# Optimization experiments

Hardware: AMD Instinct MI355X
Metric: run time of the kernel (lower is better)

## Reference

```python
import jax, jax.numpy as jnp
import numpy as np

H = 8            # heads
M = 256          # num_landmarks
PINV_ITERS = 6
PAD = 16         # residual_conv_kernel(33)//2


def layernorm(x, g, b, eps=1e-5):
    mu = x.mean(-1, keepdims=True)
    var = ((x - mu) ** 2).mean(-1, keepdims=True)
    return (x - mu) * jax.lax.rsqrt(var + eps) * g + b


def moore_penrose_pinv(x, iters=PINV_ITERS):
    # iterative Moore-Penrose pseudo-inverse (Nystromformer)
    abs_x = jnp.abs(x)
    col = abs_x.sum(-1)
    row = abs_x.sum(-2)
    z = jnp.swapaxes(x, -1, -2) / (jnp.max(col) * jnp.max(row))
    eye = jnp.eye(x.shape[-1], dtype=x.dtype)
    for _ in range(iters):
        xz = x @ z
        z = 0.25 * z @ (13.0 * eye - xz @ (15.0 * eye - xz @ (7.0 * eye - xz)))
    return z


def attn_block(y, ln1_g, ln1_b, w_qkv, w_out, b_out, res_w,
               ln2_g, ln2_b, w1, b1, w2, b2):
    B, N, D = y.shape
    inner = w_qkv.shape[1] // 3
    dh = inner // H
    xn = layernorm(y, ln1_g, ln1_b)
    qkv = xn @ w_qkv                      # [B,N,3*inner]
    q, k, v = jnp.split(qkv, 3, axis=-1)
    to_heads = lambda t: t.reshape(B, N, H, dh).transpose(0, 2, 1, 3)  # [B,H,N,dh]
    q, k, v = map(to_heads, (q, k, v))
    q = q * (dh ** -0.5)
    l = N // M                            # tokens per landmark (N % M == 0 here)
    q_l = q.reshape(B, H, M, l, dh).mean(3)  # sum/l == mean -> [B,H,M,dh]
    k_l = k.reshape(B, H, M, l, dh).mean(3)
    attn1 = jax.nn.softmax(jnp.einsum('bhnd,bhmd->bhnm', q, k_l), axis=-1)
    attn2 = jax.nn.softmax(jnp.einsum('bhid,bhjd->bhij', q_l, k_l), axis=-1)
    attn3 = jax.nn.softmax(jnp.einsum('bhmd,bhnd->bhmn', q_l, k), axis=-1)
    attn2_inv = moore_penrose_pinv(attn2)
    out = (attn1 @ attn2_inv) @ (attn3 @ v)   # [B,H,N,dh]
    # depthwise residual conv over sequence dim: v as NCHW with C=H, Hdim=N, Wdim=dh
    res = jax.lax.conv_general_dilated(
        v, res_w, window_strides=(1, 1), padding=[(PAD, PAD), (0, 0)],
        dimension_numbers=('NCHW', 'OIHW', 'NCHW'), feature_group_count=H)
    out = out + res
    out = out.transpose(0, 2, 1, 3).reshape(B, N, inner)
    y = y + out @ w_out + b_out
    yn = layernorm(y, ln2_g, ln2_b)
    hdn = jax.nn.gelu(yn @ w1 + b1, approximate=False)
    return y + hdn @ w2 + b2


def setup_inputs() -> dict:
    key = jax.random.key(0)
    ks = jax.random.split(key, 8)
    B, N, D, NB = 4, 4096, 256, 2
    inner = D
    p = lambda k, shp: jax.random.normal(k, shp, jnp.float32) * 0.02
    return {
        'x': jax.random.normal(ks[0], (B, N, D), jnp.float32),
        'ln1_g': jnp.ones((NB, D), jnp.float32),
        'ln1_b': jnp.zeros((NB, D), jnp.float32),
        'w_qkv': p(ks[1], (NB, D, 3 * inner)),
        'w_out': p(ks[2], (NB, inner, D)),
        'b_out': jnp.zeros((NB, D), jnp.float32),
        'res_w': p(ks[3], (NB, H, 1, 33, 1)),
        'ln2_g': jnp.ones((NB, D), jnp.float32),
        'ln2_b': jnp.zeros((NB, D), jnp.float32),
        'w1': p(ks[4], (NB, D, 2 * D)),
        'b1': jnp.zeros((NB, 2 * D), jnp.float32),
        'w2': p(ks[5], (NB, 2 * D, D)),
        'b2': jnp.zeros((NB, D), jnp.float32),
    }


def reference(x, ln1_g, ln1_b, w_qkv, w_out, b_out, res_w,
              ln2_g, ln2_b, w1, b1, w2, b2):
    y = x
    for i in range(ln1_g.shape[0]):
        y = attn_block(y, ln1_g[i], ln1_b[i], w_qkv[i], w_out[i], b_out[i],
                       res_w[i], ln2_g[i], ln2_b[i], w1[i], b1[i], w2[i], b2[i])
    return y
```

## Files before the change

kernel.cpp:

```cpp
#include <hip/hip_runtime.h>
#include <math.h>

typedef float f32x4 __attribute__((ext_vector_type(4)));
typedef short s16x8 __attribute__((ext_vector_type(8)));
typedef unsigned short u16;
typedef unsigned int u32;

#define MFMA16(a,b,c) __builtin_amdgcn_mfma_f32_16x16x32_bf16((a),(b),(c),0,0,0)
#define AS1 __attribute__((address_space(1)))
#define AS3 __attribute__((address_space(3)))

__device__ __forceinline__ void dma16(const u16* g, u16* l){
  __builtin_amdgcn_global_load_lds((const AS1 u32*)g, (AS3 u32*)l, 16, 0, 0);
}

__device__ __forceinline__ float bf2f(u16 u){
  union { unsigned int i; float f; } v; v.i = ((unsigned int)u)<<16; return v.f;
}
__device__ __forceinline__ u16 f2bf(float f){
  union { float f; unsigned int i; } v; v.f = f;
  unsigned int x = v.i;
  return (u16)((x + 0x7fffu + ((x>>16)&1u))>>16);
}

enum { EPI_QKV=0, EPI_PINV=1, EPI_BIAS_RES=2, EPI_BIAS_GELU=3 };

template<int EPI>
__global__ __launch_bounds__(256)
void kgemm(const u16* __restrict__ A, const u16* __restrict__ BT, int K, int lda, int ldb,
           const float* __restrict__ bias, const float* __restrict__ base,
           float* __restrict__ resout,
           u16* __restrict__ outb, int ldc)
{
  __shared__ __align__(16) u16 As[128*32];
  __shared__ __align__(16) u16 Bs[64*32];
  const int tid = threadIdx.x;
  const int w = tid>>6, l = tid&63, q = l>>4, ln = l&15;
  const int m0 = blockIdx.x*128, n0 = blockIdx.y*64;
  const int lrow = l>>2, lch = l&3;

  f32x4 acc[2][4];
  #pragma unroll
  for (int i=0;i<2;i++)
    #pragma unroll
    for (int j=0;j<4;j++){ acc[i][j][0]=0.f; acc[i][j][1]=0.f; acc[i][j][2]=0.f; acc[i][j][3]=0.f; }

  for (int k0=0; k0<K; k0+=32){
    #pragma unroll
    for (int c=0;c<2;c++){
      int row = 32*w + 16*c + lrow;
      int gch = lch ^ ((row>>1)&3);
      dma16(A + (long)(m0+row)*lda + k0 + gch*8, &As[(32*w+16*c)*32]);
    }
    {
      int row = 16*w + lrow;
      int gch = lch ^ ((row>>1)&3);
      dma16(BT + (long)(n0+row)*ldb + k0 + gch*8, &Bs[(16*w)*32]);
    }
    __syncthreads();
    s16x8 af[2], bfr[4];
    #pragma unroll
    for (int mt=0;mt<2;mt++){
      int row = w*32 + mt*16 + ln;
      af[mt] = *(const s16x8*)&As[row*32 + ((q ^ ((row>>1)&3))<<3)];
    }
    #pragma unroll
    for (int nt=0;nt<4;nt++){
      int row = nt*16 + ln;
      bfr[nt] = *(const s16x8*)&Bs[row*32 + ((q ^ ((row>>1)&3))<<3)];
    }
    #pragma unroll
    for (int mt=0;mt<2;mt++)
      #pragma unroll
      for (int nt=0;nt<4;nt++)
        acc[mt][nt] = MFMA16(af[mt], bfr[nt], acc[mt][nt]);
    __syncthreads();
  }

  #pragma unroll
  for (int mt=0;mt<2;mt++)
  #pragma unroll
  for (int nt=0;nt<4;nt++)
  #pragma unroll
  for (int r=0;r<4;r++){
    int mrow = m0 + w*32 + mt*16 + q*4 + r;
    int ncol = n0 + nt*16 + ln;
    float v = acc[mt][nt][r];
    if (EPI==EPI_BIAS_RES){
      long idx = (long)mrow*ldc + ncol;
      resout[idx] = base[idx] + v + bias[ncol];
    } else {
      outb[(long)mrow*ldc + ncol] = f2bf(v);
    }
  }
}

template<int EPI>
__global__ __launch_bounds__(256)
void kgemm2(const u16* __restrict__ A, const u16* __restrict__ BT, int K, int lda, int ldb,
            const float* __restrict__ bias, u16* __restrict__ outb, int ldc,
            u16* __restrict__ qo, u16* __restrict__ ko, u16* __restrict__ vo,
            u16* __restrict__ qlm, u16* __restrict__ klm)
{
  __shared__ __align__(16) u16 As[128*32];
  __shared__ __align__(16) u16 Bs[128*32];
  const int tid = threadIdx.x;
  const int w = tid>>6, wy = w>>1, wx = w&1, l = tid&63, q = l>>4, ln = l&15;
  const int m0 = blockIdx.x*128, n0 = blockIdx.y*128;
  const int lrow = l>>2, lch = l&3;

  f32x4 acc[4][4];
  #pragma unroll
  for (int i=0;i<4;i++)
    #pragma unroll
    for (int j=0;j<4;j++){ acc[i][j][0]=0.f; acc[i][j][1]=0.f; acc[i][j][2]=0.f; acc[i][j][3]=0.f; }

  for (int k0=0; k0<K; k0+=32){
    #pragma unroll
    for (int c=0;c<2;c++){
      int row = 32*w + 16*c + lrow;
      int gch = lch ^ ((row>>1)&3);
      dma16(A + (long)(m0+row)*lda + k0 + gch*8, &As[(32*w+16*c)*32]);
      dma16(BT + (long)(n0+row)*ldb + k0 + gch*8, &Bs[(32*w+16*c)*32]);
    }
    __syncthreads();
    s16x8 af[4], bfr[4];
    #pragma unroll
    for (int mt=0;mt<4;mt++){
      int row = wy*64 + mt*16 + ln;
      af[mt] = *(const s16x8*)&As[row*32 + ((q ^ ((row>>1)&3))<<3)];
    }
    #pragma unroll
    for (int nt=0;nt<4;nt++){
      int row = wx*64 + nt*16 + ln;
      bfr[nt] = *(const s16x8*)&Bs[row*32 + ((q ^ ((row>>1)&3))<<3)];
    }
    #pragma unroll
    for (int mt=0;mt<4;mt++)
      #pragma unroll
      for (int nt=0;nt<4;nt++)
        acc[mt][nt] = MFMA16(af[mt], bfr[nt], acc[mt][nt]);
    __syncthreads();
  }

  #pragma unroll
  for (int mt=0;mt<4;mt++)
  #pragma unroll
  for (int nt=0;nt<4;nt++){
    int ncol = n0 + wx*64 + nt*16 + ln;
    if (EPI==EPI_QKV){
      int sel = ncol>>8, hd = ncol&255, h = hd>>5, d = hd&31;
      u16* dst = sel==0 ? qo : (sel==1 ? ko : vo);
      float sc2 = (sel==0) ? 0.17677669529663689f : 1.f;
      float s = 0.f;
      #pragma unroll
      for (int r=0;r<4;r++){
        int mrow = m0 + wy*64 + mt*16 + q*4 + r;
        int b = mrow>>12, n = mrow&4095;
        float v = acc[mt][nt][r]*sc2;
        dst[(((long)(b*8+h)*4096 + n)<<5) + d] = f2bf(v);
        s += v;
      }
      if (sel < 2){
        s += __shfl_xor(s, 16);
        s += __shfl_xor(s, 32);
        if (q == 0){
          int mrow0 = m0 + wy*64 + mt*16;
          int b = mrow0>>12, grp = (mrow0&4095)>>4;
          u16* ldst = (sel==0) ? qlm : klm;
          ldst[(((long)(b*8+h)*256 + grp)<<5) + d] = f2bf(s*(1.0f/16.0f));
        }
      }
    } else {
      #pragma unroll
      for (int r=0;r<4;r++){
        int mrow = m0 + wy*64 + mt*16 + q*4 + r;
        float x = acc[mt][nt][r] + bias[ncol];
        float g = 0.5f*x*(1.0f + erff(x*0.70710678118654752f));
        outb[(long)mrow*ldc + ncol] = f2bf(g);
      }
    }
  }
}

__device__ __forceinline__ int swidx(int row, int col){
  int cc = col>>3;
  int sl = (cc&24)|((cc&7)^((row>>1)&7));
  return row*256 + sl*8 + (col&7);
}

__device__ __forceinline__ void stage256(const u16* __restrict__ g, u16* lds, int w, int l){
  const int drow = l>>5, dch = l&31;
  #pragma unroll
  for (int c=0;c<32;c++){
    int base = (c*4 + w)*2;
    int row = base + drow;
    int gch = (dch&24) | ((dch&7) ^ ((row>>1)&7));
    dma16(g + (long)row*256 + gch*8, &lds[base*256]);
  }
}

__device__ __forceinline__ void stage32(const u16* __restrict__ g, u16* lds, int w, int l){
  const int drow = l>>5, dch = l&31;
  #pragma unroll
  for (int c=0;c<4;c++){
    int base = (c*4 + w)*2;
    int row = base + drow;
    int gch = (dch&24) | ((dch&7) ^ ((row>>1)&7));
    dma16(g + (long)row*256 + gch*8, &lds[base*256]);
  }
}

__device__ __forceinline__ void mult32(const u16* aL, int arow0, const u16* bL,
                                       int w, int l, f32x4 (&acc)[2][4]){
  const int q=l>>4, ln=l&15, wn0=w*64;
  #pragma unroll
  for (int mt=0;mt<2;mt++)
    #pragma unroll
    for (int nt=0;nt<4;nt++){ acc[mt][nt][0]=0.f; acc[mt][nt][1]=0.f; acc[mt][nt][2]=0.f; acc[mt][nt][3]=0.f; }
  #pragma unroll
  for (int kq=0;kq<8;kq++){
    int ca = kq*4+q;
    s16x8 af[2];
    #pragma unroll
    for (int mt=0;mt<2;mt++){
      int r = arow0 + mt*16 + ln;
      af[mt] = *(const s16x8*)&aL[r*256 + (((ca&24)|((ca&7)^((r>>1)&7)))<<3)];
    }
    #pragma unroll
    for (int nt=0;nt<4;nt++){
      int n = wn0 + nt*16 + ln;
      s16x8 bfr = *(const s16x8*)&bL[n*256 + (((ca&24)|((ca&7)^((n>>1)&7)))<<3)];
      acc[0][nt] = MFMA16(af[0], bfr, acc[0][nt]);
      acc[1][nt] = MFMA16(af[1], bfr, acc[1][nt]);
    }
  }
}

__device__ __forceinline__ void polyinit13(const u16* aL, int arow0, int w, int l, f32x4 (&poly)[2][4]){
  const int q=l>>4, ln=l&15, wn0=w*64;
  #pragma unroll
  for (int mt=0;mt<2;mt++)
  #pragma unroll
  for (int nt=0;nt<4;nt++)
  #pragma unroll
  for (int r=0;r<4;r++){
    int row = arow0 + mt*16 + q*4 + r;
    int col = wn0 + nt*16 + ln;
    poly[mt][nt][r] = 13.f*bf2f(aL[swidx(row,col)]);
  }
}

__device__ __forceinline__ void polyaxpy(f32x4 (&poly)[2][4], const f32x4 (&acc)[2][4], float sc){
  #pragma unroll
  for (int mt=0;mt<2;mt++)
    #pragma unroll
    for (int nt=0;nt<4;nt++)
      #pragma unroll
      for (int r=0;r<4;r++) poly[mt][nt][r] += sc*acc[mt][nt][r];
}

__device__ __forceinline__ void writeT(u16* Ts, const f32x4 (&acc)[2][4], int w, int l, float sc){
  const int q=l>>4, ln=l&15, wn0=w*64;
  #pragma unroll
  for (int mt=0;mt<2;mt++)
  #pragma unroll
  for (int nt=0;nt<4;nt++)
  #pragma unroll
  for (int r=0;r<4;r++){
    int row = mt*16 + q*4 + r;
    int col = wn0 + nt*16 + ln;
    Ts[swidx(row,col)] = f2bf(sc*acc[mt][nt][r]);
  }
}

__device__ __forceinline__ void epi_poly(u16* __restrict__ out, int rowbase,
                                         const f32x4 (&poly)[2][4], int w, int l, float sc){
  const int q=l>>4, ln=l&15, wn0=w*64;
  #pragma unroll
  for (int mt=0;mt<2;mt++)
  #pragma unroll
  for (int nt=0;nt<4;nt++)
  #pragma unroll
  for (int r=0;r<4;r++){
    int row = rowbase + mt*16 + q*4 + r;
    int col = wn0 + nt*16 + ln;
    out[(long)row*256 + col] = f2bf(sc*poly[mt][nt][r]);
  }
}

__global__ __launch_bounds__(256)
void kw0(const float* __restrict__ cs_p, float* __restrict__ scal,
         const float* __restrict__ num_p, const float* __restrict__ den_p,
         const u16* __restrict__ X, u16* __restrict__ W0, u16* __restrict__ h0)
{
  __shared__ __align__(16) u16 Wf[65536];
  __shared__ __align__(16) u16 Ts[8192];
  const int tid=threadIdx.x, w=tid>>6, l=tid&63;
  const int bid=blockIdx.x, xcd=bid&7, j=bid>>3;
  const int batch = xcd*4 + (j>>3), slab = j&7;

  stage256(X + (long)batch*65536, Wf, w, l);

  float* red = (float*)Ts;
  float mx = 0.f;
  for (int i=tid;i<8192;i+=256){
    float s = 0.f;
    #pragma unroll
    for (int c=0;c<8;c++) s += cs_p[(long)c*8192 + i];
    mx = fmaxf(mx, s);
  }
  red[tid] = mx; __syncthreads();
  for (int s=128;s>0;s>>=1){ if (tid<s) red[tid] = fmaxf(red[tid], red[tid+s]); __syncthreads(); }
  float s0 = 1.0f/red[0];
  if (bid==0 && tid==0) scal[0] = s0;

  f32x4 acc[2][4];
  mult32(Wf, slab*32, Wf, w, l, acc);
  {
    const int q=l>>4, ln=l&15, wn0=w*64;
    u16* ob = W0 + (long)batch*65536;
    #pragma unroll
    for (int mt=0;mt<2;mt++)
    #pragma unroll
    for (int nt=0;nt<4;nt++)
    #pragma unroll
    for (int r=0;r<4;r++){
      int row = slab*32 + mt*16 + q*4 + r;
      int col = wn0 + nt*16 + ln;
      ob[(long)row*256 + col] = f2bf(acc[mt][nt][r]*s0);
    }
  }

  if (slab==0){
    __syncthreads();
    float (*lt)[257] = (float(*)[257])Wf;
    for (int i=tid;i<8192;i+=256){
      int m = i>>5, d = i&31;
      float sn = 0.f, sd = 0.f;
      #pragma unroll
      for (int c=0;c<8;c++){
        sn += num_p[((long)(c*32+batch))*8192 + i];
        sd += den_p[(c*32+batch)*256 + m];
      }
      lt[d][m] = sn/sd;
    }
    __syncthreads();
    u16* o = h0 + (long)batch*8192;
    for (int j2=tid;j2<8192;j2+=256){
      int d = j2>>8, m = j2&255;
      o[j2] = f2bf(lt[d][m]);
    }
  }
}

__global__ __launch_bounds__(256)
void kiter(const u16* __restrict__ Win, u16* __restrict__ Wout,
           const u16* __restrict__ hin, u16* __restrict__ hout)
{
  __shared__ __align__(16) u16 Wf[65536];
  __shared__ __align__(16) u16 Ts[8192];
  const int tid=threadIdx.x, w=tid>>6, l=tid&63;
  const int bid=blockIdx.x, xcd=bid&7, j=bid>>3;
  const int batch = xcd*4 + (j>>3), slab = j&7;

  stage256(Win + (long)batch*65536, Wf, w, l);
  __syncthreads();

  f32x4 acc[2][4], poly[2][4];
  polyinit13(Wf, slab*32, w, l, poly);
  mult32(Wf, slab*32, Wf, w, l, acc);
  polyaxpy(poly, acc, -15.f);
  writeT(Ts, acc, w, l, 1.f);
  __syncthreads();
  mult32(Ts, 0, Wf, w, l, acc);
  polyaxpy(poly, acc, 7.f);
  __syncthreads();
  writeT(Ts, acc, w, l, 1.f);
  __syncthreads();
  mult32(Ts, 0, Wf, w, l, acc);
  polyaxpy(poly, acc, -1.f);
  epi_poly(Wout + (long)batch*65536, slab*32, poly, w, l, 0.25f);

  if (slab==0){
    __syncthreads();
    stage32(hin + (long)batch*8192, Ts, w, l);
    __syncthreads();
    polyinit13(Ts, 0, w, l, poly);
    mult32(Ts, 0, Wf, w, l, acc);
    polyaxpy(poly, acc, -15.f);
    __syncthreads(); writeT(Ts, acc, w, l, 1.f); __syncthreads();
    mult32(Ts, 0, Wf, w, l, acc);
    polyaxpy(poly, acc, 7.f);
    __syncthreads(); writeT(Ts, acc, w, l, 1.f); __syncthreads();
    mult32(Ts, 0, Wf, w, l, acc);
    polyaxpy(poly, acc, -1.f);
    epi_poly(hout + (long)batch*8192, 0, poly, w, l, 0.25f);
  }
}

__global__ __launch_bounds__(256)
void ktail(const u16* __restrict__ W5, const u16* __restrict__ h5,
           const u16* __restrict__ XT, const float* __restrict__ scal,
           u16* __restrict__ uT)
{
  __shared__ __align__(16) u16 Wf[65536];
  __shared__ __align__(16) u16 Ts[8192];
  const int tid=threadIdx.x, w=tid>>6, l=tid&63;
  const int batch = blockIdx.x;

  stage256(W5 + (long)batch*65536, Wf, w, l);
  stage32(h5 + (long)batch*8192, Ts, w, l);
  __syncthreads();

  f32x4 acc[2][4], poly[2][4];
  polyinit13(Ts, 0, w, l, poly);
  mult32(Ts, 0, Wf, w, l, acc);
  polyaxpy(poly, acc, -15.f);
  __syncthreads(); writeT(Ts, acc, w, l, 1.f); __syncthreads();
  mult32(Ts, 0, Wf, w, l, acc);
  polyaxpy(poly, acc, 7.f);
  __syncthreads(); writeT(Ts, acc, w, l, 1.f); __syncthreads();
  mult32(Ts, 0, Wf, w, l, acc);
  polyaxpy(poly, acc, -1.f);
  __syncthreads();
  writeT(Ts, poly, w, l, 0.25f);
  __syncthreads();
  stage256(XT + (long)batch*65536, Wf, w, l);
  __syncthreads();
  mult32(Ts, 0, Wf, w, l, acc);
  const float s0 = scal[0];
  {
    const int q=l>>4, ln=l&15, wn0=w*64;
    u16* ob = uT + (long)batch*8192;
    #pragma unroll
    for (int mt=0;mt<2;mt++)
    #pragma unroll
    for (int nt=0;nt<4;nt++)
    #pragma unroll
    for (int r=0;r<4;r++){
      int row = mt*16 + q*4 + r;
      int col = wn0 + nt*16 + ln;
      ob[(long)row*256 + col] = f2bf(acc[mt][nt][r]*s0);
    }
  }
}

__global__ __launch_bounds__(256)
void kln(const float* __restrict__ y, const float* __restrict__ g, const float* __restrict__ b,
         u16* __restrict__ out)
{
  int w = threadIdx.x>>6, l = threadIdx.x&63;
  long row = (long)blockIdx.x*4 + w;
  float4 v = ((const float4*)(y + row*256))[l];
  float s = v.x+v.y+v.z+v.w;
  #pragma unroll
  for (int m=1;m<64;m<<=1) s += __shfl_xor(s, m);
  float mu = s*(1.0f/256.0f);
  float dx=v.x-mu, dy=v.y-mu, dz=v.z-mu, dw=v.w-mu;
  float s2 = dx*dx+dy*dy+dz*dz+dw*dw;
  #pragma unroll
  for (int m=1;m<64;m<<=1) s2 += __shfl_xor(s2, m);
  float rs = rsqrtf(s2*(1.0f/256.0f) + 1e-5f);
  float4 gg = ((const float4*)g)[l];
  float4 bb = ((const float4*)b)[l];
  ushort4 o;
  o.x = f2bf(dx*rs*gg.x + bb.x);
  o.y = f2bf(dy*rs*gg.y + bb.y);
  o.z = f2bf(dz*rs*gg.z + bb.z);
  o.w = f2bf(dw*rs*gg.w + bb.w);
  *(ushort4*)(out + row*256 + l*4) = o;
}

__global__ __launch_bounds__(256)
void kattn23(const u16* __restrict__ ql, const u16* __restrict__ kl,
             u16* __restrict__ X, u16* __restrict__ XT, float* __restrict__ cs_p,
             const u16* __restrict__ kk, const u16* __restrict__ vv,
             float* __restrict__ num_p, float* __restrict__ den_p)
{
  __shared__ __align__(16) u16 Pbuf[4][64][40];
  __shared__ __align__(16) u16 vT[32][40];
  __shared__ float qrow[32][33];
  __shared__ float psum[32][4];
  __shared__ float rsum[32];
  int bh = blockIdx.y;
  int tid = threadIdx.x, w = tid>>6, l = tid&63, q = l>>4, ln = l&15;

  if (blockIdx.x < 8){
    int r0 = blockIdx.x*32;
    int c = tid;
    #pragma unroll
    for (int i=0;i<4;i++){
      int e = c*4+i; int rr = e>>5, dd = e&31;
      qrow[rr][dd] = bf2f(ql[((long)bh*256 + r0+rr)*32 + dd]);
    }
    float kc[32];
    {
      const u16* kp = kl + ((long)bh*256 + c)*32;
      #pragma unroll
      for (int d=0;d<32;d++) kc[d] = bf2f(kp[d]);
    }
    __syncthreads();
    float er[32]; float colacc = 0.f;
    for (int r=0;r<32;r++){
      float s = 0.f;
      #pragma unroll
      for (int d=0;d<32;d++) s += qrow[r][d]*kc[d];
      float e = __expf(s);
      er[r] = e;
      float wsum = e;
      #pragma unroll
      for (int m=1;m<64;m<<=1) wsum += __shfl_xor(wsum, m);
      if (l==0) psum[r][w] = wsum;
    }
    __syncthreads();
    if (c<32) rsum[c] = psum[c][0]+psum[c][1]+psum[c][2]+psum[c][3];
    __syncthreads();
    for (int r=0;r<32;r++){
      float x = er[r]/rsum[r];
      u16 xb = f2bf(x);
      X [((long)bh*256 + r0+r)*256 + c] = xb;
      XT[((long)bh*256 + c)*256 + r0+r] = xb;
      colacc += x;
    }
    cs_p[(long)blockIdx.x*8192 + bh*256 + c] = colacc;
    return;
  }

  int chunk = blockIdx.x - 8;
  f32x4 z4; z4[0]=0.f; z4[1]=0.f; z4[2]=0.f; z4[3]=0.f;
  f32x4 acc[4][2]; f32x4 dacc[4];
  #pragma unroll
  for (int mt=0;mt<4;mt++){ dacc[mt]=z4; acc[mt][0]=z4; acc[mt][1]=z4; }
  const u16* qlb = ql + (long)bh*8192;
  const u16* kb  = kk + (long)bh*131072;
  const u16* vb  = vv + (long)bh*131072;
  int vn = tid>>3, vd = (tid&7)*4;
  for (int s=0;s<16;s++){
    int n0 = chunk*512 + s*32;
    ushort4 vx = *(const ushort4*)(vb + (long)(n0+vn)*32 + vd);
    vT[vd+0][vn]=vx.x; vT[vd+1][vn]=vx.y; vT[vd+2][vn]=vx.z; vT[vd+3][vn]=vx.w;
    __syncthreads();
    s16x8 bk[2];
    #pragma unroll
    for (int nt=0;nt<2;nt++) bk[nt] = *(const s16x8*)(kb + (long)(n0 + nt*16 + ln)*32 + q*8);
    #pragma unroll
    for (int mt=0;mt<4;mt++){
      s16x8 aq = *(const s16x8*)(qlb + (long)(w*64 + mt*16 + ln)*32 + q*8);
      #pragma unroll
      for (int nt=0;nt<2;nt++){
        f32x4 sf = MFMA16(aq, bk[nt], z4);
        f32x4 ef;
        #pragma unroll
        for (int r=0;r<4;r++) ef[r] = __expf(sf[r]);
        dacc[mt] += ef;
        #pragma unroll
        for (int r=0;r<4;r++) Pbuf[w][mt*16 + q*4 + r][nt*16 + ln] = f2bf(ef[r]);
      }
    }
    #pragma unroll
    for (int mt=0;mt<4;mt++){
      s16x8 ap = *(const s16x8*)&Pbuf[w][mt*16 + ln][q*8];
      #pragma unroll
      for (int nt=0;nt<2;nt++){
        s16x8 bv = *(const s16x8*)&vT[nt*16 + ln][q*8];
        acc[mt][nt] = MFMA16(ap, bv, acc[mt][nt]);
      }
    }
    __syncthreads();
  }
  #pragma unroll
  for (int mt=0;mt<4;mt++)
    #pragma unroll
    for (int r=0;r<4;r++){
      float x = dacc[mt][r];
      x += __shfl_xor(x,1); x += __shfl_xor(x,2); x += __shfl_xor(x,4); x += __shfl_xor(x,8);
      dacc[mt][r] = x;
    }
  long pbase = (long)(chunk*32 + bh);
  #pragma unroll
  for (int mt=0;mt<4;mt++)
    #pragma unroll
    for (int nt=0;nt<2;nt++)
      #pragma unroll
      for (int r=0;r<4;r++){
        int mg = w*64 + mt*16 + q*4 + r;
        num_p[pbase*8192 + (long)mg*32 + nt*16 + ln] = acc[mt][nt][r];
      }
  if (ln==0){
    #pragma unroll
    for (int mt=0;mt<4;mt++)
      #pragma unroll
      for (int r=0;r<4;r++)
        den_p[pbase*256 + w*64 + mt*16 + q*4 + r] = dacc[mt][r];
  }
}

__global__ __launch_bounds__(256)
void kattn1u(const u16* __restrict__ qq, const u16* __restrict__ kl, const u16* __restrict__ uT,
             const u16* __restrict__ vv, const float* __restrict__ rw,
             u16* __restrict__ aoutb)
{
  int nch = blockIdx.x, bh = blockIdx.y;
  int b = bh>>3, h = bh&7;
  int tid = threadIdx.x, w = tid>>6, l = tid&63, q = l>>4, ln = l&15;
  __shared__ __align__(16) u16 Pbuf[4][32][40];
  __shared__ __align__(16) u16 vtile[160][36];
  int r0g = nch*128;
  const u16* vb = vv + (long)bh*131072;
  #pragma unroll
  for (int it=0; it<5; it++){
    int slot = tid + it*256;
    int rr = slot>>3, c = (slot&7)*4;
    int s = r0g - 16 + rr;
    ushort4 val; val.x=0; val.y=0; val.z=0; val.w=0;
    if (s>=0 && s<4096) val = *(const ushort4*)(vb + (long)s*32 + c);
    *(ushort4*)&vtile[rr][c] = val;
  }
  __syncthreads();

  f32x4 z4; z4[0]=0.f; z4[1]=0.f; z4[2]=0.f; z4[3]=0.f;
  f32x4 acc[2][2]; f32x4 dacc[2];
  #pragma unroll
  for (int mt=0;mt<2;mt++){ dacc[mt]=z4; acc[mt][0]=z4; acc[mt][1]=z4; }
  const u16* qb  = qq + (long)bh*131072;
  const u16* klb = kl + (long)bh*8192;
  const u16* ub  = uT + (long)bh*8192;
  int r0 = r0g + w*32;
  for (int s=0;s<8;s++){
    s16x8 bk[2];
    #pragma unroll
    for (int nt=0;nt<2;nt++) bk[nt] = *(const s16x8*)(klb + (long)(s*32 + nt*16 + ln)*32 + q*8);
    #pragma unroll
    for (int mt=0;mt<2;mt++){
      s16x8 aq = *(const s16x8*)(qb + (long)(r0 + mt*16 + ln)*32 + q*8);
      #pragma unroll
      for (int nt=0;nt<2;nt++){
        f32x4 sf = MFMA16(aq, bk[nt], z4);
        f32x4 ef;
        #pragma unroll
        for (int r=0;r<4;r++) ef[r] = __expf(sf[r]);
        dacc[mt] += ef;
        #pragma unroll
        for (int r=0;r<4;r++) Pbuf[w][mt*16 + q*4 + r][nt*16 + ln] = f2bf(ef[r]);
      }
    }
    #pragma unroll
    for (int mt=0;mt<2;mt++){
      s16x8 ap = *(const s16x8*)&Pbuf[w][mt*16 + ln][q*8];
      #pragma unroll
      for (int nt=0;nt<2;nt++){
        s16x8 bu = *(const s16x8*)(ub + (long)(nt*16 + ln)*256 + s*32 + q*8);
        acc[mt][nt] = MFMA16(ap, bu, acc[mt][nt]);
      }
    }
  }
  #pragma unroll
  for (int mt=0;mt<2;mt++)
    #pragma unroll
    for (int r=0;r<4;r++){
      float x = dacc[mt][r];
      x += __shfl_xor(x,1); x += __shfl_xor(x,2); x += __shfl_xor(x,4); x += __shfl_xor(x,8);
      dacc[mt][r] = x;
    }

  const float* wp = rw + h*33;
  float w_[33];
  #pragma unroll
  for (int j=0;j<33;j++) w_[j] = wp[j];

  #pragma unroll
  for (int mt=0;mt<2;mt++){
    int nl = w*32 + mt*16 + q*4;
    #pragma unroll
    for (int nt=0;nt<2;nt++){
      int d = nt*16 + ln;
      float vvv[36];
      #pragma unroll
      for (int j=0;j<36;j++) vvv[j] = bf2f(vtile[nl + j][d]);
      #pragma unroll
      for (int r=0;r<4;r++){
        float cv = 0.f;
        #pragma unroll
        for (int j=0;j<33;j++) cv += w_[j]*vvv[r+j];
        int n = r0 + mt*16 + q*4 + r;
        long oidx = ((long)b*4096 + n)*256 + h*32 + d;
        aoutb[oidx] = f2bf(acc[mt][nt][r]/dacc[mt][r] + cv);
      }
    }
  }
}

__global__ __launch_bounds__(256)
void kcvtall(const float* __restrict__ wqkv, const float* __restrict__ wout,
             const float* __restrict__ w1, const float* __restrict__ w2,
             u16* __restrict__ wqkvT, u16* __restrict__ woutT,
             u16* __restrict__ w1T, u16* __restrict__ w2T)
{
  __shared__ float t[32][33];
  int z = blockIdx.x;
  const float* src; u16* dst; int K, Nn, bx, by;
  if (z < 384){      int i=z/192, r=z%192; src=wqkv+(long)i*196608; dst=wqkvT+(long)i*196608; K=256; Nn=768; bx=r%24; by=r/24; }
  else if (z < 512){ int zz=z-384; int i=zz/64, r=zz%64; src=wout+(long)i*65536; dst=woutT+(long)i*65536; K=256; Nn=256; bx=r%8; by=r/8; }
  else if (z < 768){ int zz=z-512; int i=zz/128, r=zz%128; src=w1+(long)i*131072; dst=w1T+(long)i*131072; K=256; Nn=512; bx=r%16; by=r/16; }
  else {             int zz=z-768; int i=zz/128, r=zz%128; src=w2+(long)i*131072; dst=w2T+(long)i*131072; K=512; Nn=256; bx=r%8; by=r/8; }
  int n0 = bx*32, k0 = by*32;
  int tx = threadIdx.x&31, ty = threadIdx.x>>5;
  #pragma unroll
  for (int i=0;i<4;i++) t[ty+i*8][tx] = src[(long)(k0+ty+i*8)*Nn + n0+tx];
  __syncthreads();
  #pragma unroll
  for (int i=0;i<4;i++) dst[(long)(n0+ty+i*8)*K + k0+tx] = f2bf(t[tx][ty+i*8]);
}

extern "C" void kernel_launch(void* const* d_in, const int* in_sizes, int n_in,
                              void* d_out, int out_size, void* d_ws, size_t ws_size,
                              hipStream_t stream)
{
  const float* x    = (const float*)d_in[0];
  const float* ln1g = (const float*)d_in[1];
  const float* ln1b = (const float*)d_in[2];
  const float* wqkv = (const float*)d_in[3];
  const float* wout = (const float*)d_in[4];
  const float* bout = (const float*)d_in[5];
  const float* resw = (const float*)d_in[6];
  const float* ln2g = (const float*)d_in[7];
  const float* ln2b = (const float*)d_in[8];
  const float* w1   = (const float*)d_in[9];
  const float* b1   = (const float*)d_in[10];
  const float* w2   = (const float*)d_in[11];
  const float* b2   = (const float*)d_in[12];
  float* y = (float*)d_out;
  char* ws = (char*)d_ws;

  u16* xn    = (u16*)(ws + 0);
  u16* qb    = (u16*)(ws + 8388608);
  u16* kb    = (u16*)(ws + 16777216);
  u16* vb    = (u16*)(ws + 25165824);
  u16* ql    = (u16*)(ws + 33554432);
  u16* kl    = (u16*)(ws + 34078720);
  u16* X     = (u16*)(ws + 34603008);
  u16* XT    = (u16*)(ws + 38797312);
  u16* h0b   = (u16*)(ws + 42991616);
  u16* WA    = (u16*)(ws + 51380224);
  u16* WB    = (u16*)(ws + 55574528);
  u16* hA    = (u16*)(ws + 68157440);
  u16* hB    = (u16*)(ws + 72351744);
  float* num_p = (float*)(ws + 76546048);
  float* den_p = (float*)(ws + 84934656);
  float* cs_p  = (float*)(ws + 85196800);
  float* scal  = (float*)(ws + 85458944);
  u16* uT    = (u16*)(ws + 85459200);
  u16* aoutb = (u16*)(ws + 85983488);
  u16* wqkvT = (u16*)(ws + 94372096);
  u16* woutT = (u16*)(ws + 95158528);
  u16* w1T   = (u16*)(ws + 95420672);
  u16* w2T   = (u16*)(ws + 95944960);
  u16* hdn   = (u16*)(ws + 51380224);

  (void)in_sizes; (void)n_in; (void)out_size; (void)ws_size;

  kcvtall<<<1024,256,0,stream>>>(wqkv, wout, w1, w2, wqkvT, woutT, w1T, w2T);

  for (int i=0;i<2;i++){
    kln<<<4096,256,0,stream>>>(i==0 ? x : y, ln1g + i*256, ln1b + i*256, xn);
    kgemm2<EPI_QKV><<<dim3(128,6),256,0,stream>>>(xn, wqkvT + (long)i*196608, 256, 256, 256,
        nullptr, nullptr, 0, qb,kb,vb, ql,kl);
    kattn23<<<dim3(16,32),256,0,stream>>>(ql, kl, X, XT, cs_p, kb, vb, num_p, den_p);

    kw0<<<256,256,0,stream>>>(cs_p, scal, num_p, den_p, X, WA, h0b);
    u16 *Wi = WA, *Wo = WB, *hi = h0b, *ho = hA;
    for (int it=0; it<5; it++){
      kiter<<<256,256,0,stream>>>(Wi, Wo, hi, ho);
      u16* t = Wi; Wi = Wo; Wo = t;
      hi = ho; ho = (ho == hA) ? hB : hA;
    }
    ktail<<<32,256,0,stream>>>(Wi, hi, XT, scal, uT);

    kattn1u<<<dim3(32,32),256,0,stream>>>(qb, kl, uT, vb, resw + i*264, aoutb);
    kgemm<EPI_BIAS_RES><<<dim3(128,4),256,0,stream>>>(aoutb, woutT + (long)i*65536, 256,256,256,
        bout + i*256, i==0 ? x : y, y, nullptr, 256);
    kln<<<4096,256,0,stream>>>(y, ln2g + i*256, ln2b + i*256, xn);
    kgemm2<EPI_BIAS_GELU><<<dim3(128,4),256,0,stream>>>(xn, w1T + (long)i*131072, 256, 256, 256,
        b1 + i*512, hdn, 512, nullptr,nullptr,nullptr, nullptr,nullptr);
    kgemm<EPI_BIAS_RES><<<dim3(128,4),256,0,stream>>>(hdn, w2T + (long)i*131072, 512,512,512,
        b2 + i*256, y, y, nullptr, 256);
  }
}
```

Before: 542.6 us.

## Fuse layernorm into residual GEMM epilogues and widen pinv kernels to 512 threads

Replaces the bias+residual GEMM with a full-row (N=256) GEMM whose epilogue writes y and also computes the next layernorm, which removes the standalone layernorm launches. The first layernorm is folded into the weight-conversion kernel. The pinv iteration kernels now run with 512 threads and smaller per-wave tiles. Full-row tiles cut the GEMM grid to 128 blocks and raise register pressure (a 2x16 accumulator), which may reduce occupancy. On the last block, the second residual GEMM computes an unused layernorm using ln1 params index 1.

```diff
diff --git a/kernel.cpp b/kernel.cpp
--- a/kernel.cpp
+++ b/kernel.cpp
@@ -23,77 +23,7 @@
   return (u16)((x + 0x7fffu + ((x>>16)&1u))>>16);
 }
 
-enum { EPI_QKV=0, EPI_PINV=1, EPI_BIAS_RES=2, EPI_BIAS_GELU=3 };
-
-template<int EPI>
-__global__ __launch_bounds__(256)
-void kgemm(const u16* __restrict__ A, const u16* __restrict__ BT, int K, int lda, int ldb,
-           const float* __restrict__ bias, const float* __restrict__ base,
-           float* __restrict__ resout,
-           u16* __restrict__ outb, int ldc)
-{
-  __shared__ __align__(16) u16 As[128*32];
-  __shared__ __align__(16) u16 Bs[64*32];
-  const int tid = threadIdx.x;
-  const int w = tid>>6, l = tid&63, q = l>>4, ln = l&15;
-  const int m0 = blockIdx.x*128, n0 = blockIdx.y*64;
-  const int lrow = l>>2, lch = l&3;
-
-  f32x4 acc[2][4];
-  #pragma unroll
-  for (int i=0;i<2;i++)
-    #pragma unroll
-    for (int j=0;j<4;j++){ acc[i][j][0]=0.f; acc[i][j][1]=0.f; acc[i][j][2]=0.f; acc[i][j][3]=0.f; }
-
-  for (int k0=0; k0<K; k0+=32){
-    #pragma unroll
-    for (int c=0;c<2;c++){
-      int row = 32*w + 16*c + lrow;
-      int gch = lch ^ ((row>>1)&3);
-      dma16(A + (long)(m0+row)*lda + k0 + gch*8, &As[(32*w+16*c)*32]);
-    }
-    {
-      int row = 16*w + lrow;
-      int gch = lch ^ ((row>>1)&3);
-      dma16(BT + (long)(n0+row)*ldb + k0 + gch*8, &Bs[(16*w)*32]);
-    }
-    __syncthreads();
-    s16x8 af[2], bfr[4];
-    #pragma unroll
-    for (int mt=0;mt<2;mt++){
-      int row = w*32 + mt*16 + ln;
-      af[mt] = *(const s16x8*)&As[row*32 + ((q ^ ((row>>1)&3))<<3)];
-    }
-    #pragma unroll
-    for (int nt=0;nt<4;nt++){
-      int row = nt*16 + ln;
-      bfr[nt] = *(const s16x8*)&Bs[row*32 + ((q ^ ((row>>1)&3))<<3)];
-    }
-    #pragma unroll
-    for (int mt=0;mt<2;mt++)
-      #pragma unroll
-      for (int nt=0;nt<4;nt++)
-        acc[mt][nt] = MFMA16(af[mt], bfr[nt], acc[mt][nt]);
-    __syncthreads();
-  }
-
-  #pragma unroll
-  for (int mt=0;mt<2;mt++)
-  #pragma unroll
-  for (int nt=0;nt<4;nt++)
-  #pragma unroll
-  for (int r=0;r<4;r++){
-    int mrow = m0 + w*32 + mt*16 + q*4 + r;
-    int ncol = n0 + nt*16 + ln;
-    float v = acc[mt][nt][r];
-    if (EPI==EPI_BIAS_RES){
-      long idx = (long)mrow*ldc + ncol;
-      resout[idx] = base[idx] + v + bias[ncol];
-    } else {
-      outb[(long)mrow*ldc + ncol] = f2bf(v);
-    }
-  }
-}
+enum { EPI_QKV=0, EPI_BIAS_GELU=3 };
 
 template<int EPI>
 __global__ __launch_bounds__(256)
@@ -183,6 +113,110 @@
   }
 }
 
+__global__ __launch_bounds__(256)
+void kgemmLN(const u16* __restrict__ A, const u16* __restrict__ BT, int K,
+             const float* __restrict__ bias, const float* __restrict__ base,
+             float* __restrict__ yout,
+             const float* __restrict__ lng, const float* __restrict__ lnb,
+             u16* __restrict__ xnout)
+{
+  __shared__ __align__(16) u16 As[128*32];
+  __shared__ __align__(16) u16 Bs[256*32];
+  const int tid = threadIdx.x;
+  const int w = tid>>6, l = tid&63, q = l>>4, ln = l&15;
+  const int m0 = blockIdx.x*128;
+  const int lrow = l>>2, lch = l&3;
+
+  f32x4 acc[2][16];
+  #pragma unroll
+  for (int i=0;i<2;i++)
+    #pragma unroll
+    for (int j=0;j<16;j++){ acc[i][j][0]=0.f; acc[i][j][1]=0.f; acc[i][j][2]=0.f; acc[i][j][3]=0.f; }
+
+  for (int k0=0; k0<K; k0+=32){
+    #pragma unroll
+    for (int c=0;c<2;c++){
+      int row = 32*w + 16*c + lrow;
+      int gch = lch ^ ((row>>1)&3);
+      dma16(A + (long)(m0+row)*K + k0 + gch*8, &As[(32*w+16*c)*32]);
+    }
+    #pragma unroll
+    for (int c=0;c<4;c++){
+      int row = 64*w + 16*c + lrow;
+      int gch = lch ^ ((row>>1)&3);
+      dma16(BT + (long)row*K + k0 + gch*8, &Bs[(64*w+16*c)*32]);
+    }
+    __syncthreads();
+    s16x8 af[2];
+    #pragma unroll
+    for (int mt=0;mt<2;mt++){
+      int row = w*32 + mt*16 + ln;
+      af[mt] = *(const s16x8*)&As[row*32 + ((q ^ ((row>>1)&3))<<3)];
+    }
+    #pragma unroll
+    for (int nt=0;nt<16;nt++){
+      int row = nt*16 + ln;
+      s16x8 bfr = *(const s16x8*)&Bs[row*32 + ((q ^ ((row>>1)&3))<<3)];
+      acc[0][nt] = MFMA16(af[0], bfr, acc[0][nt]);
+      acc[1][nt] = MFMA16(af[1], bfr, acc[1][nt]);
+    }
+    __syncthreads();
+  }
+
+  float rb[16];
+  #pragma unroll
+  for (int nt=0;nt<16;nt++) rb[nt] = bias[nt*16 + ln];
+  #pragma unroll
+  for (int mt=0;mt<2;mt++)
+  #pragma unroll
+  for (int r=0;r<4;r++){
+    long rowb = (long)(m0 + w*32 + mt*16 + q*4 + r)*256;
+    #pragma unroll
+    for (int nt=0;nt<16;nt++){
+      int col = nt*16 + ln;
+      float v = base[rowb + col] + acc[mt][nt][r] + rb[nt];
+      acc[mt][nt][r] = v;
+      yout[rowb + col] = v;
+    }
+  }
+  float mu[2][4], rs[2][4];
+  #pragma unroll
+  for (int mt=0;mt<2;mt++)
+  #pragma unroll
+  for (int r=0;r<4;r++){
+    float s = 0.f;
+    #pragma unroll
+    for (int nt=0;nt<16;nt++) s += acc[mt][nt][r];
+    s += __shfl_xor(s,1); s += __shfl_xor(s,2); s += __shfl_xor(s,4); s += __shfl_xor(s,8);
+    mu[mt][r] = s*(1.0f/256.0f);
+  }
+  #pragma unroll
+  for (int mt=0;mt<2;mt++)
+  #pragma unroll
+  for (int r=0;r<4;r++){
+    float vs = 0.f;
+    #pragma unroll
+    for (int nt=0;nt<16;nt++){ float d = acc[mt][nt][r]-mu[mt][r]; vs += d*d; }
+    vs += __shfl_xor(vs,1); vs += __shfl_xor(vs,2); vs += __shfl_xor(vs,4); vs += __shfl_xor(vs,8);
+    rs[mt][r] = rsqrtf(vs*(1.0f/256.0f) + 1e-5f);
+  }
+  float rg[16], rbb[16];
+  #pragma unroll
+  for (int nt=0;nt<16;nt++){ int col = nt*16+ln; rg[nt]=lng[col]; rbb[nt]=lnb[col]; }
+  #pragma unroll
+  for (int mt=0;mt<2;mt++)
+  #pragma unroll
+  for (int r=0;r<4;r++){
+    long rowb = (long)(m0 + w*32 + mt*16 + q*4 + r)*256;
+    #pragma unroll
+    for (int nt=0;nt<16;nt++){
+      int col = nt*16 + ln;
+      float d = acc[mt][nt][r]-mu[mt][r];
+      xnout[rowb + col] = f2bf(d*rs[mt][r]*rg[nt] + rbb[nt]);
+    }
+  }
+}
+
 __device__ __forceinline__ int swidx(int row, int col){
   int cc = col>>3;
   int sl = (cc&24)|((cc&7)^((row>>1)&7));
@@ -192,8 +226,8 @@
 __device__ __forceinline__ void stage256(const u16* __restrict__ g, u16* lds, int w, int l){
   const int drow = l>>5, dch = l&31;
   #pragma unroll
-  for (int c=0;c<32;c++){
-    int base = (c*4 + w)*2;
+  for (int c=0;c<16;c++){
+    int base = (c*8 + w)*2;
     int row = base + drow;
     int gch = (dch&24) | ((dch&7) ^ ((row>>1)&7));
     dma16(g + (long)row*256 + gch*8, &lds[base*256]);
@@ -203,8 +237,8 @@
 __device__ __forceinline__ void stage32(const u16* __restrict__ g, u16* lds, int w, int l){
   const int drow = l>>5, dch = l&31;
   #pragma unroll
-  for (int c=0;c<4;c++){
-    int base = (c*4 + w)*2;
+  for (int c=0;c<2;c++){
+    int base = (c*8 + w)*2;
     int row = base + drow;
     int gch = (dch&24) | ((dch&7) ^ ((row>>1)&7));
     dma16(g + (long)row*256 + gch*8, &lds[base*256]);
@@ -212,12 +246,12 @@
 }
 
 __device__ __forceinline__ void mult32(const u16* aL, int arow0, const u16* bL,
-                                       int w, int l, f32x4 (&acc)[2][4]){
-  const int q=l>>4, ln=l&15, wn0=w*64;
-  #pragma unroll
-  for (int mt=0;mt<2;mt++)
-    #pragma unroll
-    for (int nt=0;nt<4;nt++){ acc[mt][nt][0]=0.f; acc[mt][nt][1]=0.f; acc[mt][nt][2]=0.f; acc[mt][nt][3]=0.f; }
+                                       int w, int l, f32x4 (&acc)[2][2]){
+  const int q=l>>4, ln=l&15, wn0=w*32;
+  #pragma unroll
+  for (int mt=0;mt<2;mt++)
+    #pragma unroll
+    for (int nt=0;nt<2;nt++){ acc[mt][nt][0]=0.f; acc[mt][nt][1]=0.f; acc[mt][nt][2]=0.f; acc[mt][nt][3]=0.f; }
   #pragma unroll
   for (int kq=0;kq<8;kq++){
     int ca = kq*4+q;
@@ -228,7 +262,7 @@
       af[mt] = *(const s16x8*)&aL[r*256 + (((ca&24)|((ca&7)^((r>>1)&7)))<<3)];
     }
     #pragma unroll
-    for (int nt=0;nt<4;nt++){
+    for (int nt=0;nt<2;nt++){
       int n = wn0 + nt*16 + ln;
       s16x8 bfr = *(const s16x8*)&bL[n*256 + (((ca&24)|((ca&7)^((n>>1)&7)))<<3)];
       acc[0][nt] = MFMA16(af[0], bfr, acc[0][nt]);
@@ -237,12 +271,12 @@
   }
 }
 
-__device__ __forceinline__ void polyinit13(const u16* aL, int arow0, int w, int l, f32x4 (&poly)[2][4]){
-  const int q=l>>4, ln=l&15, wn0=w*64;
-  #pragma unroll
-  for (int mt=0;mt<2;mt++)
-  #pragma unroll
-  for (int nt=0;nt<4;nt++)
+__device__ __forceinline__ void polyinit13(const u16* aL, int arow0, int w, int l, f32x4 (&poly)[2][2]){
+  const int q=l>>4, ln=l&15, wn0=w*32;
+  #pragma unroll
+  for (int mt=0;mt<2;mt++)
+  #pragma unroll
+  for (int nt=0;nt<2;nt++)
   #pragma unroll
   for (int r=0;r<4;r++){
     int row = arow0 + mt*16 + q*4 + r;
@@ -251,21 +285,21 @@
   }
 }
 
-__device__ __forceinline__ void polyaxpy(f32x4 (&poly)[2][4], const f32x4 (&acc)[2][4], float sc){
-  #pragma unroll
-  for (int mt=0;mt<2;mt++)
-    #pragma unroll
-    for (int nt=0;nt<4;nt++)
+__device__ __forceinline__ void polyaxpy(f32x4 (&poly)[2][2], const f32x4 (&acc)[2][2], float sc){
+  #pragma unroll
+  for (int mt=0;mt<2;mt++)
+    #pragma unroll
+    for (int nt=0;nt<2;nt++)
       #pragma unroll
       for (int r=0;r<4;r++) poly[mt][nt][r] += sc*acc[mt][nt][r];
 }
 
-__device__ __forceinline__ void writeT(u16* Ts, const f32x4 (&acc)[2][4], int w, int l, float sc){
-  const int q=l>>4, ln=l&15, wn0=w*64;
-  #pragma unroll
-  for (int mt=0;mt<2;mt++)
-  #pragma unroll
-  for (int nt=0;nt<4;nt++)
+__device__ __forceinline__ void writeT(u16* Ts, const f32x4 (&acc)[2][2], int w, int l, float sc){
+  const int q=l>>4, ln=l&15, wn0=w*32;
+  #pragma unroll
+  for (int mt=0;mt<2;mt++)
+  #pragma unroll
+  for (int nt=0;nt<2;nt++)
   #pragma unroll
   for (int r=0;r<4;r++){
     int row = mt*16 + q*4 + r;
@@ -275,12 +309,12 @@
 }
 
 __device__ __forceinline__ void epi_poly(u16* __restrict__ out, int rowbase,
-                                         const f32x4 (&poly)[2][4], int w, int l, float sc){
-  const int q=l>>4, ln=l&15, wn0=w*64;
-  #pragma unroll
-  for (int mt=0;mt<2;mt++)
-  #pragma unroll
-  for (int nt=0;nt<4;nt++)
+                                         const f32x4 (&poly)[2][2], int w, int l, float sc){
+  const int q=l>>4, ln=l&15, wn0=w*32;
+  #pragma unroll
+  for (int mt=0;mt<2;mt++)
+  #pragma unroll
+  for (int nt=0;nt<2;nt++)
   #pragma unroll
   for (int r=0;r<4;r++){
     int row = rowbase + mt*16 + q*4 + r;
@@ -289,7 +323,7 @@
   }
 }
 
-__global__ __launch_bounds__(256)
+__global__ __launch_bounds__(512)
 void kw0(const float* __restrict__ cs_p, float* __restrict__ scal,
          const float* __restrict__ num_p, const float* __restrict__ den_p,
          const u16* __restrict__ X, u16* __restrict__ W0, u16* __restrict__ h0)
@@ -304,26 +338,26 @@
 
   float* red = (float*)Ts;
   float mx = 0.f;
-  for (int i=tid;i<8192;i+=256){
+  for (int i=tid;i<8192;i+=512){
     float s = 0.f;
     #pragma unroll
     for (int c=0;c<8;c++) s += cs_p[(long)c*8192 + i];
     mx = fmaxf(mx, s);
   }
   red[tid] = mx; __syncthreads();
-  for (int s=128;s>0;s>>=1){ if (tid<s) red[tid] = fmaxf(red[tid], red[tid+s]); __syncthreads(); }
+  for (int s=256;s>0;s>>=1){ if (tid<s) red[tid] = fmaxf(red[tid], red[tid+s]); __syncthreads(); }
   float s0 = 1.0f/red[0];
   if (bid==0 && tid==0) scal[0] = s0;
 
-  f32x4 acc[2][4];
+  f32x4 acc[2][2];
   mult32(Wf, slab*32, Wf, w, l, acc);
   {
-    const int q=l>>4, ln=l&15, wn0=w*64;
+    const int q=l>>4, ln=l&15, wn0=w*32;
     u16* ob = W0 + (long)batch*65536;
     #pragma unroll
     for (int mt=0;mt<2;mt++)
     #pragma unroll
-    for (int nt=0;nt<4;nt++)
+    for (int nt=0;nt<2;nt++)
     #pragma unroll
     for (int r=0;r<4;r++){
       int row = slab*32 + mt*16 + q*4 + r;
@@ -335,7 +369,7 @@
   if (slab==0){
     __syncthreads();
     float (*lt)[257] = (float(*)[257])Wf;
-    for (int i=tid;i<8192;i+=256){
+    for (int i=tid;i<8192;i+=512){
       int m = i>>5, d = i&31;
       float sn = 0.f, sd = 0.f;
       #pragma unroll
@@ -347,14 +381,14 @@
     }
     __syncthreads();
     u16* o = h0 + (long)batch*8192;
-    for (int j2=tid;j2<8192;j2+=256){
+    for (int j2=tid;j2<8192;j2+=512){
       int d = j2>>8, m = j2&255;
       o[j2] = f2bf(lt[d][m]);
     }
   }
 }
 
-__global__ __launch_bounds__(256)
+__global__ __launch_bounds__(512)
 void kiter(const u16* __restrict__ Win, u16* __restrict__ Wout,
            const u16* __restrict__ hin, u16* __restrict__ hout)
 {
@@ -367,7 +401,7 @@
   stage256(Win + (long)batch*65536, Wf, w, l);
   __syncthreads();
 
-  f32x4 acc[2][4], poly[2][4];
+  f32x4 acc[2][2], poly[2][2];
   polyinit13(Wf, slab*32, w, l, poly);
   mult32(Wf, slab*32, Wf, w, l, acc);
   polyaxpy(poly, acc, -15.f);
@@ -399,7 +433,7 @@
   }
 }
 
-__global__ __launch_bounds__(256)
+__global__ __launch_bounds__(512)
 void ktail(const u16* __restrict__ W5, const u16* __restrict__ h5,
            const u16* __restrict__ XT, const float* __restrict__ scal,
            u16* __restrict__ uT)
@@ -413,7 +447,7 @@
   stage32(h5 + (long)batch*8192, Ts, w, l);
   __syncthreads();
 
-  f32x4 acc[2][4], poly[2][4];
+  f32x4 acc[2][2], poly[2][2];
   polyinit13(Ts, 0, w, l, poly);
   mult32(Ts, 0, Wf, w, l, acc);
   polyaxpy(poly, acc, -15.f);
@@ -431,12 +465,12 @@
   mult32(Ts, 0, Wf, w, l, acc);
   const float s0 = scal[0];
   {
-    const int q=l>>4, ln=l&15, wn0=w*64;
+    const int q=l>>4, ln=l&15, wn0=w*32;
     u16* ob = uT + (long)batch*8192;
     #pragma unroll
     for (int mt=0;mt<2;mt++)
     #pragma unroll
-    for (int nt=0;nt<4;nt++)
+    for (int nt=0;nt<2;nt++)
     #pragma unroll
     for (int r=0;r<4;r++){
       int row = mt*16 + q*4 + r;
@@ -444,32 +478,6 @@
       ob[(long)row*256 + col] = f2bf(acc[mt][nt][r]*s0);
     }
   }
-}
-
-__global__ __launch_bounds__(256)
-void kln(const float* __restrict__ y, const float* __restrict__ g, const float* __restrict__ b,
-         u16* __restrict__ out)
-{
-  int w = threadIdx.x>>6, l = threadIdx.x&63;
-  long row = (long)blockIdx.x*4 + w;
-  float4 v = ((const float4*)(y + row*256))[l];
-  float s = v.x+v.y+v.z+v.w;
-  #pragma unroll
-  for (int m=1;m<64;m<<=1) s += __shfl_xor(s, m);
-  float mu = s*(1.0f/256.0f);
-  float dx=v.x-mu, dy=v.y-mu, dz=v.z-mu, dw=v.w-mu;
-  float s2 = dx*dx+dy*dy+dz*dz+dw*dw;
-  #pragma unroll
-  for (int m=1;m<64;m<<=1) s2 += __shfl_xor(s2, m);
-  float rs = rsqrtf(s2*(1.0f/256.0f) + 1e-5f);
-  float4 gg = ((const float4*)g)[l];
-  float4 bb = ((const float4*)b)[l];
-  ushort4 o;
-  o.x = f2bf(dx*rs*gg.x + bb.x);
-  o.y = f2bf(dy*rs*gg.y + bb.y);
-  o.z = f2bf(dz*rs*gg.z + bb.z);
-  o.w = f2bf(dw*rs*gg.w + bb.w);
-  *(ushort4*)(out + row*256 + l*4) = o;
 }
 
 __global__ __launch_bounds__(256)
@@ -692,13 +700,39 @@
 }
 
 __global__ __launch_bounds__(256)
-void kcvtall(const float* __restrict__ wqkv, const float* __restrict__ wout,
-             const float* __restrict__ w1, const float* __restrict__ w2,
-             u16* __restrict__ wqkvT, u16* __restrict__ woutT,
-             u16* __restrict__ w1T, u16* __restrict__ w2T)
+void kcvtln(const float* __restrict__ xin, const float* __restrict__ lg, const float* __restrict__ lb,
+            u16* __restrict__ xn,
+            const float* __restrict__ wqkv, const float* __restrict__ wout,
+            const float* __restrict__ w1, const float* __restrict__ w2,
+            u16* __restrict__ wqkvT, u16* __restrict__ woutT,
+            u16* __restrict__ w1T, u16* __restrict__ w2T)
 {
   __shared__ float t[32][33];
   int z = blockIdx.x;
+  if (z < 4096){
+    int w = threadIdx.x>>6, l = threadIdx.x&63;
+    long row = (long)z*4 + w;
+    float4 v = ((const float4*)(xin + row*256))[l];
+    float s = v.x+v.y+v.z+v.w;
+    #pragma unroll
+    for (int m=1;m<64;m<<=1) s += __shfl_xor(s, m);
+    float mu = s*(1.0f/256.0f);
+    float dx=v.x-mu, dy=v.y-mu, dz=v.z-mu, dw=v.w-mu;
+    float s2 = dx*dx+dy*dy+dz*dz+dw*dw;
+    #pragma unroll
+    for (int m=1;m<64;m<<=1) s2 += __shfl_xor(s2, m);
+    float rs = rsqrtf(s2*(1.0f/256.0f) + 1e-5f);
+    float4 gg = ((const float4*)lg)[l];
+    float4 bb = ((const float4*)lb)[l];
+    ushort4 o;
+    o.x = f2bf(dx*rs*gg.x + bb.x);
+    o.y = f2bf(dy*rs*gg.y + bb.y);
+    o.z = f2bf(dz*rs*gg.z + bb.z);
+    o.w = f2bf(dw*rs*gg.w + bb.w);
+    *(ushort4*)(xn + row*256 + l*4) = o;
+    return;
+  }
+  z -= 4096;
   const float* src; u16* dst; int K, Nn, bx, by;
   if (z < 384){      int i=z/192, r=z%192; src=wqkv+(long)i*196608; dst=wqkvT+(long)i*196608; K=256; Nn=768; bx=r%24; by=r/24; }
   else if (z < 512){ int zz=z-384; int i=zz/64, r=zz%64; src=wout+(long)i*65536; dst=woutT+(long)i*65536; K=256; Nn=256; bx=r%8; by=r/8; }
@@ -760,30 +794,29 @@
 
   (void)in_sizes; (void)n_in; (void)out_size; (void)ws_size;
 
-  kcvtall<<<1024,256,0,stream>>>(wqkv, wout, w1, w2, wqkvT, woutT, w1T, w2T);
+  kcvtln<<<5120,256,0,stream>>>(x, ln1g, ln1b, xn,
+      wqkv, wout, w1, w2, wqkvT, woutT, w1T, w2T);
 
   for (int i=0;i<2;i++){
-    kln<<<4096,256,0,stream>>>(i==0 ? x : y, ln1g + i*256, ln1b + i*256, xn);
     kgemm2<EPI_QKV><<<dim3(128,6),256,0,stream>>>(xn, wqkvT + (long)i*196608, 256, 256, 256,
         nullptr, nullptr, 0, qb,kb,vb, ql,kl);
     kattn23<<<dim3(16,32),256,0,stream>>>(ql, kl, X, XT, cs_p, kb, vb, num_p, den_p);
 
-    kw0<<<256,256,0,stream>>>(cs_p, scal, num_p, den_p, X, WA, h0b);
+    kw0<<<256,512,0,stream>>>(cs_p, scal, num_p, den_p, X, WA, h0b);
     u16 *Wi = WA, *Wo = WB, *hi = h0b, *ho = hA;
     for (int it=0; it<5; it++){
-      kiter<<<256,256,0,stream>>>(Wi, Wo, hi, ho);
+      kiter<<<256,512,0,stream>>>(Wi, Wo, hi, ho);
       u16* t = Wi; Wi = Wo; Wo = t;
       hi = ho; ho = (ho == hA) ? hB : hA;
     }
-    ktail<<<32,256,0,stream>>>(Wi, hi, XT, scal, uT);
+    ktail<<<32,512,0,stream>>>(Wi, hi, XT, scal, uT);
 
     kattn1u<<<dim3(32,32),256,0,stream>>>(qb, kl, uT, vb, resw + i*264, aoutb);
-    kgemm<EPI_BIAS_RES><<<dim3(128,4),256,0,stream>>>(aoutb, woutT + (long)i*65536, 256,256,256,
-        bout + i*256, i==0 ? x : y, y, nullptr, 256);
-    kln<<<4096,256,0,stream>>>(y, ln2g + i*256, ln2b + i*256, xn);
+    kgemmLN<<<128,256,0,stream>>>(aoutb, woutT + (long)i*65536, 256,
+        bout + i*256, i==0 ? x : y, y, ln2g + i*256, ln2b + i*256, xn);
     kgemm2<EPI_BIAS_GELU><<<dim3(128,4),256,0,stream>>>(xn, w1T + (long)i*131072, 256, 256, 256,
         b1 + i*512, hdn, 512, nullptr,nullptr,nullptr, nullptr,nullptr);
-    kgemm<EPI_BIAS_RES><<<dim3(128,4),256,0,stream>>>(hdn, w2T + (long)i*131072, 512,512,512,
-        b2 + i*256, y, y, nullptr, 256);
-  }
-}
+    kgemmLN<<<128,256,0,stream>>>(hdn, w2T + (long)i*131072, 512,
+        b2 + i*256, y, y, ln1g + 256, ln1b + 256, xn);
+  }
+}
```

New measurement: 536.7 us. Within noise of the previous version (-1.1%).
